# Kernel optimization log

Hardware: AMD Instinct MI355X
Metric: run time of the kernel (lower is better)

Reference implementation:

```python
import jax, jax.numpy as jnp
import numpy as np


def _inside_quad(pts9, quads):
    """Ray-casting point-in-polygon test (semantics of the pointsJf CUDA kernel),
    evaluated only for matched (diagonal) point/box pairs.

    pts9:  [N, 9, 2] points
    quads: [N, 8] polygon corners (x1,y1,x2,y2,x3,y3,x4,y4)
    returns inside flag [N, 9] float32 in {0.0, 1.0}
    """
    vx = quads[:, 0::2][:, None, :]          # [N,1,4]
    vy = quads[:, 1::2][:, None, :]          # [N,1,4]
    vxj = jnp.roll(vx, 1, axis=-1)           # previous vertex (j = i-1 mod 4)
    vyj = jnp.roll(vy, 1, axis=-1)
    px = pts9[..., 0:1]                      # [N,9,1]
    py = pts9[..., 1:2]                      # [N,9,1]
    straddles = (vy > py) != (vyj > py)      # edge crosses horizontal ray
    # x coordinate of edge at height py (only meaningful where straddles)
    x_int = (vxj - vx) * (py - vy) / (vyj - vy) + vx
    crossings = straddles & (px < x_int)     # [N,9,4] bool
    inside = (jnp.sum(crossings.astype(jnp.int32), axis=-1) % 2)
    return inside.astype(jnp.float32)        # [N,9]


def _spatial_border_loss(pts, gt_bboxes, weight, loss_weight):
    n = pts.shape[0]
    pts9 = pts.reshape(n, 9, 2)
    inside = _inside_quad(pts9, gt_bboxes)                    # [N,9]
    out_mask = (inside == 0.0).astype(pts.dtype)              # points outside their gt box
    cx = (gt_bboxes[:, 0] + gt_bboxes[:, 4]) * 0.5
    cy = (gt_bboxes[:, 1] + gt_bboxes[:, 5]) * 0.5
    center = jnp.stack([cx, cy], axis=1)[:, None, :]          # [N,1,2]
    dist = 0.2 * jnp.sqrt(jnp.sum((pts9 - center) ** 2, axis=-1))  # [N,9]
    cnt = jnp.sum(out_mask)
    loss_sb = jnp.where(cnt > 0, jnp.sum(dist * out_mask) / jnp.maximum(cnt, 1.0), 0.0)
    # weighted_spatial_border_loss: avg_factor = sum(weight_repeated4 > 0)/4 + 1e-6
    avg_factor = jnp.sum((weight > 0).astype(jnp.float32)) + 1e-6
    return loss_weight * (loss_sb / avg_factor)[None]          # shape [1]


def setup_inputs() -> dict:
    key = jax.random.key(0)
    k1, k2, k3 = jax.random.split(key, 3)
    N = 1_000_000
    pts = jax.random.normal(k1, (N, 18), dtype=jnp.float32)
    gt_bboxes = jax.random.normal(k2, (N, 8), dtype=jnp.float32)
    weight = jax.random.uniform(k3, (N,), dtype=jnp.float32)
    return {"pts": pts, "gt_bboxes": gt_bboxes, "weight": weight}


def reference(pts, gt_bboxes, weight):
    return _spatial_border_loss(pts, gt_bboxes, weight, loss_weight=1.0)
```

## Files before the change

### kernel.cpp

```cpp
#include <hip/hip_runtime.h>
#include <cstdint>


#define SBL_BLOCK 512
#define SBL_TILE  512
#define SBL_WAVES (SBL_BLOCK / 64)
#define SBL_CHUNKS (SBL_TILE * 72 / 1024)

__global__ void __launch_bounds__(SBL_BLOCK) sbl_main(
    const float* __restrict__ pts,
    const float* __restrict__ quads,
    const float* __restrict__ weight,
    double* __restrict__ part_sum,
    unsigned int* __restrict__ part_cnt,
    unsigned int* __restrict__ part_wpos,
    int n)
{
    __shared__ __align__(16) float s_pts[SBL_TILE * 18];

    const int tid  = threadIdx.x;
    const int lane = tid & 63;
    const int wave = tid >> 6;
    const int base = blockIdx.x * SBL_TILE;
    int rows = n - base; if (rows > SBL_TILE) rows = SBL_TILE;
    const bool have_row = (tid < rows);

    if (rows == SBL_TILE) {
        const char* gbase = (const char*)(pts + (size_t)base * 18);
        const uint32_t lds0 = (uint32_t)(uintptr_t)(void*)s_pts;
        #pragma unroll
        for (int c = 0; c < (SBL_CHUNKS + SBL_WAVES - 1) / SBL_WAVES; ++c) {
            const int chunk = wave + SBL_WAVES * c;
            if (chunk < SBL_CHUNKS) {
                const char* g = gbase + chunk * 1024 + lane * 16;
                __builtin_amdgcn_global_load_lds(
                    (const __attribute__((address_space(1))) void*)(uintptr_t)g,
                    (__attribute__((address_space(3))) void*)(uintptr_t)(lds0 + chunk * 1024 + lane * 16),
                    16, 0, 0);
            }
        }
    } else {
        const float2* g2 = reinterpret_cast<const float2*>(pts + (size_t)base * 18);
        float2* s2 = reinterpret_cast<float2*>(s_pts);
        const int nf2 = rows * 9;
        for (int idx = tid; idx < nf2; idx += SBL_BLOCK) s2[idx] = g2[idx];
    }

    float4 qa = make_float4(0.f, 0.f, 0.f, 0.f);
    float4 qb = make_float4(0.f, 0.f, 0.f, 0.f);
    float wv = 0.0f;
    if (have_row) {
        const float4* q4 = reinterpret_cast<const float4*>(quads) + (size_t)(base + tid) * 2;
        qa = q4[0];
        qb = q4[1];
        wv = weight[base + tid];
    }
    __syncthreads();

    float local_sum = 0.0f;
    unsigned int local_cnt = 0u;
    unsigned int local_wpos = (wv > 0.0f) ? 1u : 0u;

    if (have_row) {
        const float vx0 = qa.x, vy0 = qa.y, vx1 = qa.z, vy1 = qa.w;
        const float vx2 = qb.x, vy2 = qb.y, vx3 = qb.z, vy3 = qb.w;
        const float cx = (vx0 + vx2) * 0.5f;
        const float cy = (vy0 + vy2) * 0.5f;
        const float d0 = vy3 - vy0, d1 = vy0 - vy1, d2 = vy1 - vy2, d3 = vy2 - vy3;
        const float e0 = vx3 - vx0, e1 = vx0 - vx1, e2 = vx1 - vx2, e3 = vx2 - vx3;
        const bool  n0 = d0 < 0.0f, n1 = d1 < 0.0f, n2 = d2 < 0.0f, n3 = d3 < 0.0f;

        const float2* prow = reinterpret_cast<const float2*>(s_pts + tid * 18);
        #pragma unroll
        for (int k = 0; k < 9; ++k) {
            const float2 p = prow[k];
            const float px = p.x, py = p.y;

            const bool c0 = vy0 > py, c1 = vy1 > py, c2 = vy2 > py, c3 = vy3 > py;
            const bool s0 = c0 != c3, s1 = c1 != c0, s2 = c2 != c1, s3 = c3 != c2;

            const float t0 = py - vy0, t1 = py - vy1, t2 = py - vy2, t3 = py - vy3;
            const float m0 = e0 * t0, m1 = e1 * t1, m2 = e2 * t2, m3 = e3 * t3;
            const float l0 = (px - vx0) * d0, l1 = (px - vx1) * d1;
            const float l2 = (px - vx2) * d2, l3 = (px - vx3) * d3;

            const bool x0 = s0 && ((l0 < m0) != n0);
            const bool x1 = s1 && ((l1 < m1) != n1);
            const bool x2 = s2 && ((l2 < m2) != n2);
            const bool x3 = s3 && ((l3 < m3) != n3);

            const bool inside = (x0 != x1) != (x2 != x3);
            if (!inside) {
                const float dx = px - cx;
                const float dy = py - cy;
                local_sum += sqrtf(fmaf(dx, dx, dy * dy));
                local_cnt += 1u;
            }
        }
    }

    #pragma unroll
    for (int off = 32; off > 0; off >>= 1) {
        local_sum  += __shfl_down(local_sum, off, 64);
        local_cnt  += __shfl_down(local_cnt, off, 64);
        local_wpos += __shfl_down(local_wpos, off, 64);
    }

    __shared__ float        r_sum[SBL_WAVES];
    __shared__ unsigned int r_cnt[SBL_WAVES];
    __shared__ unsigned int r_wpos[SBL_WAVES];
    if (lane == 0) { r_sum[wave] = local_sum; r_cnt[wave] = local_cnt; r_wpos[wave] = local_wpos; }
    __syncthreads();
    if (tid == 0) {
        double bsum = 0.0;
        unsigned int bcnt = 0u, bwpos = 0u;
        #pragma unroll
        for (int i = 0; i < SBL_WAVES; ++i) { bsum += (double)r_sum[i]; bcnt += r_cnt[i]; bwpos += r_wpos[i]; }
        part_sum[blockIdx.x]  = bsum;
        part_cnt[blockIdx.x]  = bcnt;
        part_wpos[blockIdx.x] = bwpos;
    }
}

__global__ void __launch_bounds__(1024) sbl_finalize(
    const double* __restrict__ part_sum,
    const unsigned int* __restrict__ part_cnt,
    const unsigned int* __restrict__ part_wpos,
    float* __restrict__ out,
    int nblocks)
{
    const int tid = threadIdx.x;
    double s = 0.0;
    unsigned int c = 0u, w = 0u;
    for (int i = tid; i < nblocks; i += 1024) {
        s += part_sum[i];
        c += part_cnt[i];
        w += part_wpos[i];
    }
    #pragma unroll
    for (int off = 32; off > 0; off >>= 1) {
        s += __shfl_down(s, off, 64);
        c += __shfl_down(c, off, 64);
        w += __shfl_down(w, off, 64);
    }
    __shared__ double       fs[16];
    __shared__ unsigned int fc[16], fw[16];
    const int lane = tid & 63, wave = tid >> 6;
    if (lane == 0) { fs[wave] = s; fc[wave] = c; fw[wave] = w; }
    __syncthreads();
    if (tid == 0) {
        double ts = 0.0; unsigned int tc = 0u, tw = 0u;
        #pragma unroll
        for (int k = 0; k < 16; ++k) { ts += fs[k]; tc += fc[k]; tw += fw[k]; }
        const double loss_sb = (tc > 0u) ? (0.2 * ts / (double)tc) : 0.0;
        const double avg_factor = (double)tw + 1e-6;
        out[0] = (float)(loss_sb / avg_factor);
    }
}

extern "C" void kernel_launch(void* const* d_in, const int* in_sizes, int n_in,
                              void* d_out, int out_size, void* d_ws, size_t ws_size,
                              hipStream_t stream) {
    const float* pts    = (const float*)d_in[0];
    const float* quads  = (const float*)d_in[1];
    const float* weight = (const float*)d_in[2];
    float* out = (float*)d_out;

    const int n = in_sizes[2];
    const int nblocks = (n + SBL_TILE - 1) / SBL_TILE;

    double*       part_sum  = (double*)d_ws;
    unsigned int* part_cnt  = (unsigned int*)((char*)d_ws + (size_t)nblocks * sizeof(double));
    unsigned int* part_wpos = (unsigned int*)((char*)d_ws + (size_t)nblocks * (sizeof(double) + sizeof(unsigned int)));

    sbl_main<<<nblocks, SBL_BLOCK, 0, stream>>>(pts, quads, weight,
                                                part_sum, part_cnt, part_wpos, n);
    sbl_finalize<<<1, 1024, 0, stream>>>(part_sum, part_cnt, part_wpos, out, nblocks);
}
```

Measured before the change: 133.8 us.

## Make each wave load its own rows to LDS and drop block barrier

Rewrites the async global-to-LDS staging so each wave loads exactly the 64 rows it will consume: four 16-byte chunks plus two 4-byte tails. This lets the full-tile path replace the block-wide barrier with a per-wave wait on outstanding memory ops. It also packs the outside-count and positive-weight count into one 32-bit value, which removes one shuffle per reduction step and one shared array. The risk is that 16-bit fields could overflow, though per-wave counts stay small, and that correctness depends on LDS-DMA completion being covered by vmcnt.

Result: no change. 133.3 us (-0.4%).

```diff
diff --git a/kernel.cpp b/kernel.cpp
--- a/kernel.cpp
+++ b/kernel.cpp
@@ -5,7 +5,7 @@
 #define SBL_BLOCK 512
 #define SBL_TILE  512
 #define SBL_WAVES (SBL_BLOCK / 64)
-#define SBL_CHUNKS (SBL_TILE * 72 / 1024)
+#define SBL_WAVE_BYTES (64 * 72)
 
 __global__ void __launch_bounds__(SBL_BLOCK) sbl_main(
     const float* __restrict__ pts,
@@ -24,20 +24,26 @@
     const int base = blockIdx.x * SBL_TILE;
     int rows = n - base; if (rows > SBL_TILE) rows = SBL_TILE;
     const bool have_row = (tid < rows);
+    const bool full = (rows == SBL_TILE);
 
-    if (rows == SBL_TILE) {
-        const char* gbase = (const char*)(pts + (size_t)base * 18);
-        const uint32_t lds0 = (uint32_t)(uintptr_t)(void*)s_pts;
+    if (full) {
+        const char* g0 = (const char*)pts + (size_t)base * 72
+                       + (size_t)wave * SBL_WAVE_BYTES;
+        const uint32_t l0 = (uint32_t)(uintptr_t)(void*)s_pts
+                          + (uint32_t)(wave * SBL_WAVE_BYTES);
         #pragma unroll
-        for (int c = 0; c < (SBL_CHUNKS + SBL_WAVES - 1) / SBL_WAVES; ++c) {
-            const int chunk = wave + SBL_WAVES * c;
-            if (chunk < SBL_CHUNKS) {
-                const char* g = gbase + chunk * 1024 + lane * 16;
-                __builtin_amdgcn_global_load_lds(
-                    (const __attribute__((address_space(1))) void*)(uintptr_t)g,
-                    (__attribute__((address_space(3))) void*)(uintptr_t)(lds0 + chunk * 1024 + lane * 16),
-                    16, 0, 0);
-            }
+        for (int i = 0; i < 4; ++i) {
+            __builtin_amdgcn_global_load_lds(
+                (const __attribute__((address_space(1))) void*)(g0 + i * 1024 + lane * 16),
+                (__attribute__((address_space(3))) void*)(uintptr_t)(l0 + i * 1024 + lane * 16),
+                16, 0, 0);
+        }
+        #pragma unroll
+        for (int j = 0; j < 2; ++j) {
+            __builtin_amdgcn_global_load_lds(
+                (const __attribute__((address_space(1))) void*)(g0 + 4096 + j * 256 + lane * 4),
+                (__attribute__((address_space(3))) void*)(uintptr_t)(l0 + 4096 + j * 256 + lane * 4),
+                4, 0, 0);
         }
     } else {
         const float2* g2 = reinterpret_cast<const float2*>(pts + (size_t)base * 18);
@@ -55,11 +61,16 @@
         qb = q4[1];
         wv = weight[base + tid];
     }
-    __syncthreads();
+
+    if (full) {
+        asm volatile("s_waitcnt vmcnt(0) lgkmcnt(0)" ::: "memory");
+        __builtin_amdgcn_sched_barrier(0);
+    } else {
+        __syncthreads();
+    }
 
     float local_sum = 0.0f;
-    unsigned int local_cnt = 0u;
-    unsigned int local_wpos = (wv > 0.0f) ? 1u : 0u;
+    unsigned int pack = (wv > 0.0f) ? (1u << 16) : 0u;
 
     if (have_row) {
         const float vx0 = qa.x, vy0 = qa.y, vx1 = qa.z, vy1 = qa.w;
@@ -94,28 +105,30 @@
                 const float dx = px - cx;
                 const float dy = py - cy;
                 local_sum += sqrtf(fmaf(dx, dx, dy * dy));
-                local_cnt += 1u;
+                pack += 1u;
             }
         }
     }
 
     #pragma unroll
     for (int off = 32; off > 0; off >>= 1) {
-        local_sum  += __shfl_down(local_sum, off, 64);
-        local_cnt  += __shfl_down(local_cnt, off, 64);
-        local_wpos += __shfl_down(local_wpos, off, 64);
+        local_sum += __shfl_down(local_sum, off, 64);
+        pack      += __shfl_down(pack, off, 64);
     }
 
     __shared__ float        r_sum[SBL_WAVES];
-    __shared__ unsigned int r_cnt[SBL_WAVES];
-    __shared__ unsigned int r_wpos[SBL_WAVES];
-    if (lane == 0) { r_sum[wave] = local_sum; r_cnt[wave] = local_cnt; r_wpos[wave] = local_wpos; }
+    __shared__ unsigned int r_pack[SBL_WAVES];
+    if (lane == 0) { r_sum[wave] = local_sum; r_pack[wave] = pack; }
     __syncthreads();
     if (tid == 0) {
         double bsum = 0.0;
         unsigned int bcnt = 0u, bwpos = 0u;
         #pragma unroll
-        for (int i = 0; i < SBL_WAVES; ++i) { bsum += (double)r_sum[i]; bcnt += r_cnt[i]; bwpos += r_wpos[i]; }
+        for (int i = 0; i < SBL_WAVES; ++i) {
+            bsum  += (double)r_sum[i];
+            bcnt  += r_pack[i] & 0xffffu;
+            bwpos += r_pack[i] >> 16;
+        }
         part_sum[blockIdx.x]  = bsum;
         part_cnt[blockIdx.x]  = bcnt;
         part_wpos[blockIdx.x] = bwpos;
```
